# Optimization experiments

Hardware: AMD Instinct MI355X
Metric: run time of the kernel (lower is better)

## Reference

```python
import jax, jax.numpy as jnp
import numpy as np

K = 10
NUM_BLKS = 6
LN_EPS = 1e-6
NODE_D = 64


def layer_norm(x, g, b):
    m = jnp.mean(x, axis=-1, keepdims=True)
    v = jnp.var(x, axis=-1, keepdims=True)
    return (x - m) * jax.lax.rsqrt(v + LN_EPS) * g + b


def setup_inputs() -> dict:
    key = jax.random.key(0)
    B, N_c, N_t, D_S, D_F = 4, 4096, 1024, 3, 4
    D_IN = 4 + D_S + D_F  # obs-embed(4) + s + f
    ks = jax.random.split(key, 32)
    sc = 0.02
    inp = {
        "s_ctx": jax.random.normal(ks[0], (B, N_c, D_S), jnp.float32),
        "f_ctx": jax.random.normal(ks[1], (B, N_c, D_F), jnp.float32),
        "s_test": jax.random.normal(ks[2], (B, N_t, D_S), jnp.float32),
        "valid_lens_ctx": jax.random.randint(ks[3], (B,), N_c // 2, N_c + 1).astype(jnp.int32),
        # embed_obs: nn.Embed(2, 4)
        "emb_obs": jax.random.normal(ks[4], (2, 4), jnp.float32) * sc,
        # embed_all: MLP([256,128,64], gelu)
        "ea_W0": jax.random.normal(ks[5], (D_IN, 256), jnp.float32) * sc, "ea_b0": jnp.zeros((256,), jnp.float32),
        "ea_W1": jax.random.normal(ks[6], (256, 128), jnp.float32) * sc, "ea_b1": jnp.zeros((128,), jnp.float32),
        "ea_W2": jax.random.normal(ks[7], (128, NODE_D), jnp.float32) * sc, "ea_b2": jnp.zeros((NODE_D,), jnp.float32),
        # top-level LayerNorm
        "ln_g": jnp.ones((NODE_D,), jnp.float32), "ln_b": jnp.zeros((NODE_D,), jnp.float32),
        # GraphKRBlock params, stacked over NUM_BLKS blocks
        "blk_Wm0": jax.random.normal(ks[8], (NUM_BLKS, NODE_D + 1, 128), jnp.float32) * sc,
        "blk_bm0": jnp.zeros((NUM_BLKS, 128), jnp.float32),
        "blk_Wm1": jax.random.normal(ks[9], (NUM_BLKS, 128, NODE_D), jnp.float32) * sc,
        "blk_bm1": jnp.zeros((NUM_BLKS, NODE_D), jnp.float32),
        "blk_Wu0": jax.random.normal(ks[10], (NUM_BLKS, 2 * NODE_D, 128), jnp.float32) * sc,
        "blk_bu0": jnp.zeros((NUM_BLKS, 128), jnp.float32),
        "blk_Wu1": jax.random.normal(ks[11], (NUM_BLKS, 128, NODE_D), jnp.float32) * sc,
        "blk_bu1": jnp.zeros((NUM_BLKS, NODE_D), jnp.float32),
        "blk_lng": jnp.ones((NUM_BLKS, NODE_D), jnp.float32),
        "blk_lnb": jnp.zeros((NUM_BLKS, NODE_D), jnp.float32),
        # head: MLP([256,64,2], gelu)
        "hd_W0": jax.random.normal(ks[12], (NODE_D, 256), jnp.float32) * sc, "hd_b0": jnp.zeros((256,), jnp.float32),
        "hd_W1": jax.random.normal(ks[13], (256, 64), jnp.float32) * sc, "hd_b1": jnp.zeros((64,), jnp.float32),
        "hd_W2": jax.random.normal(ks[14], (64, 2), jnp.float32) * sc, "hd_b2": jnp.zeros((2,), jnp.float32),
    }
    return inp


def reference(s_ctx, f_ctx, s_test, valid_lens_ctx,
              emb_obs, ea_W0, ea_b0, ea_W1, ea_b1, ea_W2, ea_b2, ln_g, ln_b,
              blk_Wm0, blk_bm0, blk_Wm1, blk_bm1, blk_Wu0, blk_bu0, blk_Wu1, blk_bu1,
              blk_lng, blk_lnb, hd_W0, hd_b0, hd_W1, hd_b1, hd_W2, hd_b2):
    B, N_c, _ = s_ctx.shape
    N_t = s_test.shape[1]

    # --- per-sample O(n^2) KNN graph build (custom_k_nearest_senders, l2 dist) ---
    mask = jnp.arange(N_c)[None, :] < valid_lens_ctx[:, None]          # [B,N_c]
    s_send = jnp.where(mask[..., None], s_ctx, 1e6)                    # invalid -> far away
    rx = jnp.concatenate([s_ctx, s_test], axis=1)                      # [B,N,d_s] receivers
    d = jnp.sqrt(jnp.sum((rx[:, :, None, :] - s_send[:, None, :, :]) ** 2, axis=-1))  # [B,N,N_c]
    negd, senders = jax.lax.top_k(-d, K)                               # k-nearest: [B,N,K]
    dists = -negd                                                       # ascending distances

    # --- embeddings: stack(embed_obs, s, f) -> embed_all MLP -> LayerNorm ---
    def embed(x):
        h = jax.nn.gelu(x @ ea_W0 + ea_b0)
        h = jax.nn.gelu(h @ ea_W1 + ea_b1)
        h = h @ ea_W2 + ea_b2
        return layer_norm(h, ln_g, ln_b)

    ctx_in = jnp.concatenate(
        [jnp.broadcast_to(emb_obs[1], (B, N_c, emb_obs.shape[1])), s_ctx, f_ctx], axis=-1)
    test_in = jnp.concatenate(
        [jnp.broadcast_to(emb_obs[0], (B, N_t, emb_obs.shape[1])), s_test,
         jnp.zeros((B, N_t, f_ctx.shape[-1]), f_ctx.dtype)], axis=-1)
    nodes = jnp.concatenate([embed(ctx_in), embed(test_in)], axis=1)   # [B,N,64]

    # --- num_blks GraphKRBlock message-passing blocks ---
    bidx = jnp.arange(B)[:, None, None]
    w = jax.nn.softmax(-dists, axis=-1)                                # kernel weights per receiver
    for i in range(NUM_BLKS):
        sf = nodes[bidx, senders]                                      # gather senders [B,N,K,64]
        m_in = jnp.concatenate([sf, dists[..., None]], axis=-1)        # [B,N,K,65]
        m = jax.nn.gelu(m_in @ blk_Wm0[i] + blk_bm0[i]) @ blk_Wm1[i] + blk_bm1[i]
        agg = jnp.einsum('bnk,bnkd->bnd', w, m)                        # scatter-to-receivers
        u_in = jnp.concatenate([nodes, agg], axis=-1)                  # [B,N,128]
        upd = jax.nn.gelu(u_in @ blk_Wu0[i] + blk_bu0[i]) @ blk_Wu1[i] + blk_bu1[i]
        nodes = layer_norm(nodes + upd, blk_lng[i], blk_lnb[i])

    # --- head on test nodes ---
    x_t = nodes[:, N_c:, :]                                            # [B,N_t,64]
    h = jax.nn.gelu(x_t @ hd_W0 + hd_b0)
    h = jax.nn.gelu(h @ hd_W1 + hd_b1)
    f_dist = h @ hd_W2 + hd_b2                                         # [B,N_t,2]
    f_mu, f_log_var = jnp.split(f_dist, 2, axis=-1)
    f_std = jnp.exp(f_log_var / 2)                                     # min_std = 0.0
    return f_mu, f_std
```

## Files before the change

### kernel.cpp

```cpp
#include <hip/hip_runtime.h>
#include <math.h>

#define BB 4
#define NC 4096
#define NT 1024
#define NN (NC + NT)
#define NODES (BB * NN)
#define DD 64
#define KNN 10
#define NBLK 6
#define BIGF 3.0e38f
#define LM 5

typedef __attribute__((ext_vector_type(8))) short short8;
typedef __attribute__((ext_vector_type(4))) float f32x4;
typedef __attribute__((ext_vector_type(4))) int int4v;

__device__ __forceinline__ unsigned short f2bf(float f) {
    unsigned int u = __float_as_uint(f);
    unsigned int r = (u + 0x7fffu + ((u >> 16) & 1u)) >> 16;
    return (unsigned short)r;
}
__device__ __forceinline__ float bf2f(unsigned short h) {
    return __uint_as_float(((unsigned int)h) << 16);
}

__device__ __forceinline__ float gelu_f(float x) {
    const float c0 = 0.7978845608028654f;
    float x3 = x * x * x;
    float z2 = 2.0f * c0 * (x + 0.044715f * x3);
    float e = __expf(z2);
    float r = __builtin_amdgcn_rcpf(1.0f + e);
    return x - x * r;
}

__device__ __forceinline__ float wave_sum(float v) {
#pragma unroll
    for (int off = 32; off > 0; off >>= 1) v += __shfl_xor(v, off, 64);
    return v;
}

__device__ __forceinline__ f32x4 mfma_bf16(short8 a, short8 b, f32x4 c) {
    asm("v_mfma_f32_16x16x32_bf16 %0, %1, %2, %0" : "+v"(c) : "v"(a), "v"(b));
    return c;
}


__global__ __launch_bounds__(256) void k_convw(
    const float* __restrict__ Wm0, const float* __restrict__ Wm1,
    const float* __restrict__ Wu0, const float* __restrict__ Wu1,
    const float* __restrict__ bm0,
    const float* __restrict__ eW0, const float* __restrict__ eW1,
    const float* __restrict__ eW2,
    const float* __restrict__ hW0, const float* __restrict__ hW1,
    const float* __restrict__ sctx, const int* __restrict__ valid_lens,
    unsigned short* __restrict__ wtm0, unsigned short* __restrict__ wtm1p,
    unsigned short* __restrict__ wtu0, unsigned short* __restrict__ wtu1,
    float* __restrict__ wdp, float* __restrict__ bm0p,
    unsigned short* __restrict__ wte0, unsigned short* __restrict__ wte1,
    unsigned short* __restrict__ wte2,
    unsigned short* __restrict__ wth0, unsigned short* __restrict__ wth1,
    float4* __restrict__ s4)
{
    int t = blockIdx.x * 256 + threadIdx.x;
    if (t < 49152) {
        int i = t / 8192, r = t % 8192, n = r / 64, k = r % 64;
        wtm0[t] = f2bf(Wm0[(i * 65 + k) * 128 + n]);
    } else if (t < 98304) {
        int u = t - 49152;
        int i = u / 8192, r = u % 8192, n = r / 128, cp = r % 128;
        int col = ((cp & 7) << 4) | (cp >> 3);
        wtm1p[u] = f2bf(Wm1[(i * 128 + col) * 64 + n]);
    } else if (t < 196608) {
        int u = t - 98304;
        int i = u / 16384, r = u % 16384, n = r / 128, k = r % 128;
        wtu0[u] = f2bf(Wu0[(i * 128 + k) * 128 + n]);
    } else if (t < 245760) {
        int u = t - 196608;
        int i = u / 8192, r = u % 8192, n = r / 128, k = r % 128;
        wtu1[u] = f2bf(Wu1[(i * 128 + k) * 64 + n]);
    } else if (t < 246528) {
        int u = t - 245760;
        int i = u / 128, cp = u % 128;
        int col = ((cp & 7) << 4) | (cp >> 3);
        wdp[u] = Wm0[(i * 65 + 64) * 128 + col];
    } else if (t < 247296) {
        int u = t - 246528;
        int i = u / 128, cp = u % 128;
        int col = ((cp & 7) << 4) | (cp >> 3);
        bm0p[u] = bm0[i * 128 + col];
    } else if (t < 255488) {
        int u = t - 247296;
        int n = u / 32, k = u % 32;
        wte0[u] = (k < 11) ? f2bf(eW0[k * 256 + n]) : 0;
    } else if (t < 288256) {
        int u = t - 255488;
        int n = u / 256, k = u % 256;
        wte1[u] = f2bf(eW1[k * 128 + n]);
    } else if (t < 296448) {
        int u = t - 288256;
        int n = u / 128, k = u % 128;
        wte2[u] = f2bf(eW2[k * 64 + n]);
    } else if (t < 312832) {
        int u = t - 296448;
        int n = u / 64, k = u % 64;
        wth0[u] = f2bf(hW0[k * 256 + n]);
    } else if (t < 329216) {
        int u = t - 312832;
        int n = u / 256, k = u % 256;
        wth1[u] = f2bf(hW1[k * 64 + n]);
    } else if (t < 329216 + BB * NC) {
        int u = t - 329216;
        int b = u / NC, j = u % NC;
        bool ok = j < valid_lens[b];
        float x = ok ? sctx[u * 3] : 1.0e6f;
        float y = ok ? sctx[u * 3 + 1] : 1.0e6f;
        float z = ok ? sctx[u * 3 + 2] : 1.0e6f;
        s4[u] = make_float4(x, y, z, 0.0f);
    }
}

__global__ __launch_bounds__(256) void k_embed2(
    const float* __restrict__ s_ctx, const float* __restrict__ f_ctx,
    const float* __restrict__ s_test, const float* __restrict__ emb_obs,
    const unsigned short* __restrict__ WT0, const float* __restrict__ b0,
    const unsigned short* __restrict__ WT1, const float* __restrict__ b1,
    const unsigned short* __restrict__ WT2, const float* __restrict__ b2,
    const float* __restrict__ g, const float* __restrict__ bta,
    const unsigned short* __restrict__ Wm0n,
    unsigned short* __restrict__ nodes,
    unsigned short* __restrict__ Pout)
{
    __shared__ unsigned short H0[4][16 * 256];
    __shared__ unsigned short H1[4][16 * 128];
    __shared__ unsigned short XO[4][16 * 64];
    int t = threadIdx.x;
    int wave = t >> 6, lane = t & 63, lr = lane & 15, lk = lane >> 4;
    int rb = wave * 16;
    int n0 = blockIdx.x * 64;
    int bq = n0 / NN, nloc0 = n0 % NN;
    bool is_ctx = nloc0 < NC;
    int nr = nloc0 + rb + lr;
    float xv[8];
#pragma unroll
    for (int j = 0; j < 8; ++j) xv[j] = 0.0f;
    if (lk == 0) {
        const float* eb = emb_obs + (is_ctx ? 4 : 0);
        xv[0] = eb[0]; xv[1] = eb[1]; xv[2] = eb[2]; xv[3] = eb[3];
        if (is_ctx) {
            const float* sp = s_ctx + ((size_t)(bq * NC + nr)) * 3;
            const float* fp = f_ctx + ((size_t)(bq * NC + nr)) * 4;
            xv[4] = sp[0]; xv[5] = sp[1]; xv[6] = sp[2]; xv[7] = fp[0];
        } else {
            const float* sp = s_test + ((size_t)(bq * NT + nr - NC)) * 3;
            xv[4] = sp[0]; xv[5] = sp[1]; xv[6] = sp[2];
        }
    } else if (lk == 1 && is_ctx) {
        const float* fp = f_ctx + ((size_t)(bq * NC + nr)) * 4;
        xv[0] = fp[1]; xv[1] = fp[2]; xv[2] = fp[3];
    }
    short8 a;
#pragma unroll
    for (int j = 0; j < 8; ++j) a[j] = (short)f2bf(xv[j]);

    f32x4 acc0[16];
#pragma unroll
    for (int nt = 0; nt < 16; ++nt) {
        short8 bb = *(const short8*)(WT0 + (nt * 16 + lr) * 32 + lk * 8);
        f32x4 z = (f32x4){0.f, 0.f, 0.f, 0.f};
        acc0[nt] = mfma_bf16(a, bb, z);
    }
    unsigned short* h0 = &H0[wave][0];
#pragma unroll
    for (int nt = 0; nt < 16; ++nt) {
        int col = nt * 16 + lr;
        float bias = b0[col];
        int u = col >> 3;
#pragma unroll
        for (int j = 0; j < 4; ++j) {
            int row = lk * 4 + j;
            float v = gelu_f(acc0[nt][j] + bias);
            int us = (u & 16) | ((u ^ row) & 15);
            h0[row * 256 + us * 8 + (col & 7)] = f2bf(v);
        }
    }
    f32x4 acc1[8];
#pragma unroll
    for (int nt = 0; nt < 8; ++nt) acc1[nt] = (f32x4){0.f, 0.f, 0.f, 0.f};
#pragma unroll
    for (int ks = 0; ks < 8; ++ks) {
        int u = ks * 4 + lk;
        int us = (u & 16) | ((u ^ lr) & 15);
        short8 aa = *(const short8*)(&h0[lr * 256 + us * 8]);
#pragma unroll
        for (int nt = 0; nt < 8; ++nt) {
            short8 bb = *(const short8*)(WT1 + (nt * 16 + lr) * 256 + ks * 32 + lk * 8);
            acc1[nt] = mfma_bf16(aa, bb, acc1[nt]);
        }
    }
    unsigned short* h1 = &H1[wave][0];
#pragma unroll
    for (int nt = 0; nt < 8; ++nt) {
        int col = nt * 16 + lr;
        float bias = b1[col];
        int u = col >> 3;
#pragma unroll
        for (int j = 0; j < 4; ++j) {
            int row = lk * 4 + j;
            float v = gelu_f(acc1[nt][j] + bias);
            int us = (u ^ row) & 15;
            h1[row * 128 + us * 8 + (col & 7)] = f2bf(v);
        }
    }
    f32x4 acc2[4];
#pragma unroll
    for (int nt = 0; nt < 4; ++nt) acc2[nt] = (f32x4){0.f, 0.f, 0.f, 0.f};
#pragma unroll
    for (int ks = 0; ks < 4; ++ks) {
        int u = ks * 4 + lk;
        int us = (u ^ lr) & 15;
        short8 aa = *(const short8*)(&h1[lr * 128 + us * 8]);
#pragma unroll
        for (int nt = 0; nt < 4; ++nt) {
            short8 bb = *(const short8*)(WT2 + (nt * 16 + lr) * 128 + ks * 32 + lk * 8);
            acc2[nt] = mfma_bf16(aa, bb, acc2[nt]);
        }
    }
    float vals[4][4];
#pragma unroll
    for (int j = 0; j < 4; ++j)
#pragma unroll
        for (int nt = 0; nt < 4; ++nt)
            vals[j][nt] = acc2[nt][j] + b2[nt * 16 + lr];
    unsigned short* xo = &XO[wave][0];
#pragma unroll
    for (int j = 0; j < 4; ++j) {
        float s = vals[j][0] + vals[j][1] + vals[j][2] + vals[j][3];
#pragma unroll
        for (int m = 1; m < 16; m <<= 1) s += __shfl_xor(s, m, 64);
        float mean = s * (1.0f / 64.0f);
        float vs = 0.0f;
#pragma unroll
        for (int nt = 0; nt < 4; ++nt) { float d = vals[j][nt] - mean; vs += d * d; }
#pragma unroll
        for (int m = 1; m < 16; m <<= 1) vs += __shfl_xor(vs, m, 64);
        float inv = rsqrtf(vs * (1.0f / 64.0f) + 1e-6f);
        int row = lk * 4 + j;
        int node = n0 + rb + row;
#pragma unroll
        for (int nt = 0; nt < 4; ++nt) {
            int col = nt * 16 + lr;
            float o = (vals[j][nt] - mean) * inv * g[col] + bta[col];
            unsigned short ob = f2bf(o);
            nodes[(size_t)node * 64 + col] = ob;
            xo[row * 64 + ((col >> 3) ^ (row & 7)) * 8 + (col & 7)] = ob;
        }
    }
    f32x4 accP[8];
#pragma unroll
    for (int nt = 0; nt < 8; ++nt) accP[nt] = (f32x4){0.f, 0.f, 0.f, 0.f};
#pragma unroll
    for (int ks = 0; ks < 2; ++ks) {
        short8 aa = *(const short8*)(&xo[lr * 64 + ((ks * 4 + lk) ^ (lr & 7)) * 8]);
#pragma unroll
        for (int nt = 0; nt < 8; ++nt) {
            short8 bb = *(const short8*)(Wm0n + (nt * 16 + lr) * 64 + ks * 32 + lk * 8);
            accP[nt] = mfma_bf16(aa, bb, accP[nt]);
        }
    }
#pragma unroll
    for (int j = 0; j < 4; ++j) {
        int node = n0 + rb + lk * 4 + j;
        short8 ps;
#pragma unroll
        for (int nt = 0; nt < 8; ++nt) ps[nt] = (short)f2bf(accP[nt][j]);
        *(short8*)(Pout + (size_t)node * 128 + lr * 8) = ps;
    }
}

__global__ __launch_bounds__(256) void k_topk(
    const float4* __restrict__ s4, const float* __restrict__ s_ctx,
    const float* __restrict__ s_test,
    float* __restrict__ dists, int* __restrict__ senders, float* __restrict__ wout)
{
    __shared__ float cd[4 * 64 * 11];
    __shared__ float slotv[4][4][16];
    __shared__ int   sloti[4][4][16];
    __shared__ int   cnt[4][4];
    int wave = threadIdx.x >> 6;
    int lane = threadIdx.x & 63;
    int r0 = blockIdx.x * 16 + wave * 4;
    int b = r0 / NN;
    const float4* sc = s4 + (size_t)b * NC;
    float px[4], py[4], pz[4];
#pragma unroll
    for (int q = 0; q < 4; ++q) {
        int n = (r0 + q) % NN;
        const float* p = (n < NC) ? &s_ctx[(size_t)(b * NC + n) * 3]
                                  : &s_test[(size_t)(b * NT + (n - NC)) * 3];
        px[q] = p[0]; py[q] = p[1]; pz[q] = p[2];
    }
    float bq[4][LM];
#pragma unroll
    for (int q = 0; q < 4; ++q)
#pragma unroll
        for (int k = 0; k < LM; ++k) bq[q][k] = BIGF;
#pragma unroll 8
    for (int i = 0; i < 64; ++i) {
        int j = lane + (i << 6);
        float4 s = sc[j];
#pragma unroll
        for (int q = 0; q < 4; ++q) {
            float dx = px[q] - s.x, dy = py[q] - s.y, dz = pz[q] - s.z;
            float d2 = fmaf(dx, dx, fmaf(dy, dy, dz * dz));
#pragma unroll
            for (int k = LM - 1; k >= 1; --k)
                bq[q][k] = __builtin_amdgcn_fmed3f(bq[q][k - 1], bq[q][k], d2);
            bq[q][0] = fminf(bq[q][0], d2);
        }
    }
    int base = (wave * 64 + lane) * 11;
    float T[4];
#pragma unroll
    for (int q = 0; q < 4; ++q) {
#pragma unroll
        for (int k = 0; k < LM; ++k) cd[base + k] = bq[q][k];
        cd[base + LM] = BIGF;
        __builtin_amdgcn_wave_barrier();
        int head = 0;
        float Tl = BIGF;
#pragma unroll
        for (int rr = 0; rr < KNN; ++rr) {
            float v = cd[base + head];
            float mv = v;
#pragma unroll
            for (int off = 32; off > 0; off >>= 1) mv = fminf(mv, __shfl_xor(mv, off, 64));
            unsigned long long ball = __ballot(v == mv);
            int win = __ffsll(ball) - 1;
            if (lane == win) head++;
            Tl = mv;
        }
        T[q] = Tl;
    }
    if (lane < 4) cnt[wave][lane] = 0;
    __builtin_amdgcn_wave_barrier();
#pragma unroll 4
    for (int i = 0; i < 64; ++i) {
        int j = lane + (i << 6);
        float4 s = sc[j];
#pragma unroll
        for (int q = 0; q < 4; ++q) {
            float dx = px[q] - s.x, dy = py[q] - s.y, dz = pz[q] - s.z;
            float v = fmaf(dx, dx, fmaf(dy, dy, dz * dz));
            if (v <= T[q]) {
                int slot = atomicAdd(&cnt[wave][q], 1);
                if (slot < 16) { slotv[wave][q][slot] = v; sloti[wave][q][slot] = j; }
            }
        }
    }
    __builtin_amdgcn_wave_barrier();
#pragma unroll
    for (int q = 0; q < 4; ++q) {
        int count = cnt[wave][q];
        if (count > 16) count = 16;
        float e = 0.0f, d = 0.0f;
        int isel = 0, rank = 0;
        bool own = lane < count;
        if (own) {
            float myv = slotv[wave][q][lane];
            int myi = sloti[wave][q][lane];
            for (int j = 0; j < count; ++j) {
                float vj = slotv[wave][q][j];
                int ij = sloti[wave][q][j];
                rank += (vj < myv || (vj == myv && ij < myi)) ? 1 : 0;
            }
            own = rank < KNN;
            if (own) {
                isel = myi;
                d = sqrtf(myv);
                e = __expf(-d);
            }
        }
        float ssum = wave_sum(e);
        if (own) {
            size_t o = (size_t)(r0 + q) * KNN + rank;
            dists[o] = d;
            senders[o] = isel;
            wout[o] = e / ssum;
        }
    }
}

__global__ __launch_bounds__(256) void k_blk(
    const unsigned short* __restrict__ nodes_in,
    const unsigned short* __restrict__ P,
    const float* __restrict__ dists, const int* __restrict__ senders,
    const float* __restrict__ w,
    const float* __restrict__ wdp, const float* __restrict__ bm0p,
    const unsigned short* __restrict__ Wm1p,
    const float* __restrict__ bm1,
    const unsigned short* __restrict__ WTu0,
    const float* __restrict__ bu0,
    const unsigned short* __restrict__ WTu1,
    const float* __restrict__ bu1,
    const float* __restrict__ lng, const float* __restrict__ lnb,
    const unsigned short* __restrict__ Wm0n,
    const int doP,
    unsigned short* __restrict__ nodes_out,
    unsigned short* __restrict__ Pout,
    const int doHead, const int testOnly,
    const unsigned short* __restrict__ wth0,
    const float* __restrict__ hb0,
    const unsigned short* __restrict__ wth1,
    const float* __restrict__ hb1,
    const float* __restrict__ hW2, const float* __restrict__ hb2,
    float* __restrict__ out)
{
    __shared__ unsigned short X[16 * 64];
    __shared__ unsigned short G[16 * 128];
    __shared__ unsigned short AG[16 * 64];
    __shared__ unsigned short H[16 * 128];
    __shared__ unsigned short XO[16 * 64];
    __shared__ float VF[16 * 65];
    __shared__ unsigned short HH[16 * 256];
    __shared__ unsigned short HH1[16 * 72];
    __shared__ int   sidE[160];
    __shared__ float dE[160], wE[160];
    int l = threadIdx.x;
    int wave = l >> 6, lane = l & 63;
    int bid = blockIdx.x;
    int tile = testOnly ? ((bid >> 6) * 320 + 256 + (bid & 63))
                        : ((bid & 7) * 160 + (bid >> 3));
    int n0 = tile * 16;
    int b = n0 / NN;
    size_t bbase = (size_t)b * NN;
    int e0 = n0 * KNN;
    if (l < 160) {
        sidE[l] = senders[e0 + l];
        dE[l]   = dists[e0 + l];
        wE[l]   = w[e0 + l];
    }
    if (l < 128) {
        int row = l >> 3, u = l & 7;
        int4v v = *(const int4v*)(nodes_in + ((size_t)(n0 + row)) * 64 + u * 8);
        *(int4v*)(&X[row * 64 + (u ^ (row & 7)) * 8]) = v;
    }
    __syncthreads();
    float wd0 = wdp[2 * lane], wd1 = wdp[2 * lane + 1];
    float bb0 = bm0p[2 * lane], bb1 = bm0p[2 * lane + 1];
    const unsigned int* Pb = (const unsigned int*)P;
    unsigned int* G32 = (unsigned int*)G;
#pragma unroll
    for (int nn = 0; nn < 4; ++nn) {
        int n = wave * 4 + nn;
        float a0 = 0.0f, a1 = 0.0f;
#pragma unroll
        for (int k = 0; k < KNN; ++k) {
            int e = n * KNN + k;
            int sid = sidE[e];
            float dd = dE[e], ww = wE[e];
            unsigned int pr = Pb[(bbase + sid) * 64 + lane];
            float p0 = __uint_as_float(pr << 16);
            float p1 = __uint_as_float(pr & 0xFFFF0000u);
            float g0 = gelu_f(fmaf(dd, wd0, p0 + bb0));
            float g1 = gelu_f(fmaf(dd, wd1, p1 + bb1));
            a0 = fmaf(ww, g0, a0);
            a1 = fmaf(ww, g1, a1);
        }
        unsigned int pk = (unsigned int)f2bf(a0) | ((unsigned int)f2bf(a1) << 16);
        G32[n * 64 + ((lane >> 2) ^ n) * 4 + (lane & 3)] = pk;
    }
    __syncthreads();
    int lr = lane & 15, lk = lane >> 4;
    if (wave < 2) {
        f32x4 accA[2];
#pragma unroll
        for (int n2 = 0; n2 < 2; ++n2) accA[n2] = (f32x4){0.f, 0.f, 0.f, 0.f};
#pragma unroll
        for (int ks = 0; ks < 4; ++ks) {
            short8 a = *(const short8*)(&G[lr * 128 + ((ks * 4 + lk) ^ lr) * 8]);
#pragma unroll
            for (int n2 = 0; n2 < 2; ++n2) {
                int nt = wave * 2 + n2;
                short8 bb = *(const short8*)(Wm1p + (nt * 16 + lr) * 128 + ks * 32 + lk * 8);
                accA[n2] = mfma_bf16(a, bb, accA[n2]);
            }
        }
#pragma unroll
        for (int n2 = 0; n2 < 2; ++n2) {
            int col = (wave * 2 + n2) * 16 + lr;
            float bias = bm1[col];
#pragma unroll
            for (int j = 0; j < 4; ++j) {
                int row = lk * 4 + j;
                AG[row * 64 + ((col >> 3) ^ (row & 7)) * 8 + (col & 7)] =
                    f2bf(accA[n2][j] + bias);
            }
        }
    }
    __syncthreads();
    if (wave < 2) {
        f32x4 acc[4];
#pragma unroll
        for (int n4 = 0; n4 < 4; ++n4) acc[n4] = (f32x4){0.f, 0.f, 0.f, 0.f};
#pragma unroll
        for (int ks = 0; ks < 4; ++ks) {
            short8 a;
            if (ks < 2) a = *(const short8*)(&X[lr * 64 + ((ks * 4 + lk) ^ (lr & 7)) * 8]);
            else        a = *(const short8*)(&AG[lr * 64 + (((ks - 2) * 4 + lk) ^ (lr & 7)) * 8]);
#pragma unroll
            for (int n4 = 0; n4 < 4; ++n4) {
                int nt = wave * 4 + n4;
                short8 bb = *(const short8*)(WTu0 + (nt * 16 + lr) * 128 + ks * 32 + lk * 8);
                acc[n4] = mfma_bf16(a, bb, acc[n4]);
            }
        }
#pragma unroll
        for (int n4 = 0; n4 < 4; ++n4) {
            int col = (wave * 4 + n4) * 16 + lr;
            float bias = bu0[col];
#pragma unroll
            for (int j = 0; j < 4; ++j) {
                int lrow = lk * 4 + j;
                float v = gelu_f(acc[n4][j] + bias);
                H[lrow * 128 + ((col >> 3) ^ lrow) * 8 + (col & 7)] = f2bf(v);
            }
        }
    }
    __syncthreads();
    if (wave < 2) {
        f32x4 acc2[2];
#pragma unroll
        for (int n2 = 0; n2 < 2; ++n2) acc2[n2] = (f32x4){0.f, 0.f, 0.f, 0.f};
#pragma unroll
        for (int ks = 0; ks < 4; ++ks) {
            short8 a = *(const short8*)(&H[lr * 128 + ((ks * 4 + lk) ^ lr) * 8]);
#pragma unroll
            for (int n2 = 0; n2 < 2; ++n2) {
                int nt = wave * 2 + n2;
                short8 bb = *(const short8*)(WTu1 + (nt * 16 + lr) * 128 + ks * 32 + lk * 8);
                acc2[n2] = mfma_bf16(a, bb, acc2[n2]);
            }
        }
#pragma unroll
        for (int n2 = 0; n2 < 2; ++n2) {
            int col = (wave * 2 + n2) * 16 + lr;
            float bias = bu1[col];
#pragma unroll
            for (int j = 0; j < 4; ++j) {
                int row = lk * 4 + j;
                float x = bf2f(X[row * 64 + ((col >> 3) ^ (row & 7)) * 8 + (col & 7)]);
                VF[row * 65 + col] = x + acc2[n2][j] + bias;
            }
        }
    }
    __syncthreads();
    if (wave == 0) {
        float vals[4][4];
#pragma unroll
        for (int j = 0; j < 4; ++j) {
            int row = lk * 4 + j;
#pragma unroll
            for (int nt = 0; nt < 4; ++nt)
                vals[j][nt] = VF[row * 65 + nt * 16 + lr];
        }
#pragma unroll
        for (int j = 0; j < 4; ++j) {
            int row = lk * 4 + j;
            float s = vals[j][0] + vals[j][1] + vals[j][2] + vals[j][3];
#pragma unroll
            for (int mm = 1; mm < 16; mm <<= 1) s += __shfl_xor(s, mm, 64);
            float mean = s * (1.0f / 64.0f);
            float vs = 0.0f;
#pragma unroll
            for (int nt = 0; nt < 4; ++nt) { float d = vals[j][nt] - mean; vs += d * d; }
#pragma unroll
            for (int mm = 1; mm < 16; mm <<= 1) vs += __shfl_xor(vs, mm, 64);
            float inv = rsqrtf(vs * (1.0f / 64.0f) + 1e-6f);
#pragma unroll
            for (int nt = 0; nt < 4; ++nt) {
                int col = nt * 16 + lr;
                float o = (vals[j][nt] - mean) * inv * lng[col] + lnb[col];
                unsigned short ob = f2bf(o);
                nodes_out[((size_t)(n0 + row)) * 64 + col] = ob;
                XO[row * 64 + ((col >> 3) ^ (row & 7)) * 8 + (col & 7)] = ob;
            }
        }
    }
    __syncthreads();
    if (doP && wave == 1) {
        f32x4 accP[8];
#pragma unroll
        for (int nt = 0; nt < 8; ++nt) accP[nt] = (f32x4){0.f, 0.f, 0.f, 0.f};
#pragma unroll
        for (int ks = 0; ks < 2; ++ks) {
            short8 aa = *(const short8*)(&XO[lr * 64 + ((ks * 4 + lk) ^ (lr & 7)) * 8]);
#pragma unroll
            for (int nt = 0; nt < 8; ++nt) {
                short8 bb = *(const short8*)(Wm0n + (nt * 16 + lr) * 64 + ks * 32 + lk * 8);
                accP[nt] = mfma_bf16(aa, bb, accP[nt]);
            }
        }
#pragma unroll
        for (int j = 0; j < 4; ++j) {
            int node = n0 + lk * 4 + j;
            short8 ps;
#pragma unroll
            for (int nt = 0; nt < 8; ++nt) ps[nt] = (short)f2bf(accP[nt][j]);
            *(short8*)(Pout + (size_t)node * 128 + lr * 8) = ps;
        }
    }
    if (doHead && wave == 0) {
        int nloc = n0 % NN;
        int bq = n0 / NN;
#pragma unroll
        for (int half = 0; half < 2; ++half) {
            f32x4 ah[8];
#pragma unroll
            for (int nt = 0; nt < 8; ++nt) ah[nt] = (f32x4){0.f, 0.f, 0.f, 0.f};
#pragma unroll
            for (int ks = 0; ks < 2; ++ks) {
                short8 aa = *(const short8*)(&XO[lr * 64 + ((ks * 4 + lk) ^ (lr & 7)) * 8]);
#pragma unroll
                for (int nt = 0; nt < 8; ++nt) {
                    int col16 = half * 8 + nt;
                    short8 bb = *(const short8*)(wth0 + (col16 * 16 + lr) * 64 + ks * 32 + lk * 8);
                    ah[nt] = mfma_bf16(aa, bb, ah[nt]);
                }
            }
#pragma unroll
            for (int nt = 0; nt < 8; ++nt) {
                int col = (half * 8 + nt) * 16 + lr;
                float bias = hb0[col];
                int u = col >> 3;
#pragma unroll
                for (int j = 0; j < 4; ++j) {
                    int row = lk * 4 + j;
                    float v = gelu_f(ah[nt][j] + bias);
                    int us = (u & 16) | ((u ^ row) & 15);
                    HH[row * 256 + us * 8 + (col & 7)] = f2bf(v);
                }
            }
        }
        f32x4 a1h[4];
#pragma unroll
        for (int nt = 0; nt < 4; ++nt) a1h[nt] = (f32x4){0.f, 0.f, 0.f, 0.f};
#pragma unroll
        for (int ks = 0; ks < 8; ++ks) {
            int u = ks * 4 + lk;
            int us = (u & 16) | ((u ^ lr) & 15);
            short8 aa = *(const short8*)(&HH[lr * 256 + us * 8]);
#pragma unroll
            for (int nt = 0; nt < 4; ++nt) {
                short8 bb = *(const short8*)(wth1 + (nt * 16 + lr) * 256 + ks * 32 + lk * 8);
                a1h[nt] = mfma_bf16(aa, bb, a1h[nt]);
            }
        }
#pragma unroll
        for (int nt = 0; nt < 4; ++nt) {
            int col = nt * 16 + lr;
            float bias = hb1[col];
#pragma unroll
            for (int j = 0; j < 4; ++j) {
                int row = lk * 4 + j;
                HH1[row * 72 + col] = f2bf(gelu_f(a1h[nt][j] + bias));
            }
        }
        int task = lane >> 1;
        int row = task >> 1;
        int o = task & 1;
        int t2 = lane & 1;
        float pp = 0.0f;
#pragma unroll
        for (int d = 0; d < 32; ++d) {
            int dd = t2 * 32 + d;
            pp += bf2f(HH1[row * 72 + dd]) * hW2[dd * 2 + o];
        }
        pp += __shfl_xor(pp, 1, 64);
        if (t2 == 0) {
            int gg = bq * NT + (nloc - NC) + row;
            if (o == 0) out[gg] = pp + hb2[0];
            else        out[BB * NT + gg] = __expf(0.5f * (pp + hb2[1]));
        }
    }
}

extern "C" void kernel_launch(void* const* d_in, const int* in_sizes, int n_in,
                              void* d_out, int out_size, void* d_ws, size_t ws_size,
                              hipStream_t stream)
{
    (void)in_sizes; (void)n_in; (void)out_size; (void)ws_size;
    const float* s_ctx   = (const float*)d_in[0];
    const float* f_ctx   = (const float*)d_in[1];
    const float* s_test  = (const float*)d_in[2];
    const int*   valid   = (const int*)d_in[3];
    const float* emb_obs = (const float*)d_in[4];
    const float* ea_W0   = (const float*)d_in[5];
    const float* ea_b0   = (const float*)d_in[6];
    const float* ea_W1   = (const float*)d_in[7];
    const float* ea_b1   = (const float*)d_in[8];
    const float* ea_W2   = (const float*)d_in[9];
    const float* ea_b2   = (const float*)d_in[10];
    const float* ln_g    = (const float*)d_in[11];
    const float* ln_b    = (const float*)d_in[12];
    const float* blk_Wm0 = (const float*)d_in[13];
    const float* blk_bm0 = (const float*)d_in[14];
    const float* blk_Wm1 = (const float*)d_in[15];
    const float* blk_bm1 = (const float*)d_in[16];
    const float* blk_Wu0 = (const float*)d_in[17];
    const float* blk_bu0 = (const float*)d_in[18];
    const float* blk_Wu1 = (const float*)d_in[19];
    const float* blk_bu1 = (const float*)d_in[20];
    const float* blk_lng = (const float*)d_in[21];
    const float* blk_lnb = (const float*)d_in[22];
    const float* hd_W0   = (const float*)d_in[23];
    const float* hd_b0   = (const float*)d_in[24];
    const float* hd_W1   = (const float*)d_in[25];
    const float* hd_b1   = (const float*)d_in[26];
    const float* hd_W2   = (const float*)d_in[27];
    const float* hd_b2   = (const float*)d_in[28];

    char* p = (char*)d_ws;
    auto alloc = [&](size_t bytes) { char* r = p; p += (bytes + 255) & ~(size_t)255; return r; };
    unsigned short* nodesA = (unsigned short*)alloc((size_t)NODES * 64 * 2);
    unsigned short* nodesB = (unsigned short*)alloc((size_t)NODES * 64 * 2);
    unsigned short* PA     = (unsigned short*)alloc((size_t)NODES * 128 * 2);
    unsigned short* PB     = (unsigned short*)alloc((size_t)NODES * 128 * 2);
    float* dists   = (float*)alloc((size_t)NODES * KNN * 4);
    float* wbuf    = (float*)alloc((size_t)NODES * KNN * 4);
    int*   senders = (int*)alloc((size_t)NODES * KNN * 4);
    unsigned short* wtm0  = (unsigned short*)alloc((size_t)6 * 8192 * 2);
    unsigned short* wtm1p = (unsigned short*)alloc((size_t)6 * 8192 * 2);
    unsigned short* wtu0  = (unsigned short*)alloc((size_t)6 * 16384 * 2);
    unsigned short* wtu1  = (unsigned short*)alloc((size_t)6 * 8192 * 2);
    float* wdp  = (float*)alloc((size_t)6 * 128 * 4);
    float* bm0p = (float*)alloc((size_t)6 * 128 * 4);
    unsigned short* wte0 = (unsigned short*)alloc((size_t)8192 * 2);
    unsigned short* wte1 = (unsigned short*)alloc((size_t)32768 * 2);
    unsigned short* wte2 = (unsigned short*)alloc((size_t)8192 * 2);
    unsigned short* wth0 = (unsigned short*)alloc((size_t)16384 * 2);
    unsigned short* wth1 = (unsigned short*)alloc((size_t)16384 * 2);
    float4* s4 = (float4*)alloc((size_t)BB * NC * 16);

    k_convw<<<1350, 256, 0, stream>>>(
        blk_Wm0, blk_Wm1, blk_Wu0, blk_Wu1, blk_bm0,
        ea_W0, ea_W1, ea_W2, hd_W0, hd_W1, s_ctx, valid,
        wtm0, wtm1p, wtu0, wtu1, wdp, bm0p, wte0, wte1, wte2, wth0, wth1, s4);

    k_embed2<<<NODES / 64, 256, 0, stream>>>(s_ctx, f_ctx, s_test, emb_obs,
        wte0, ea_b0, wte1, ea_b1, wte2, ea_b2, ln_g, ln_b, wtm0, nodesA, PA);

    k_topk<<<NODES / 16, 256, 0, stream>>>(s4, s_ctx, s_test,
                                           dists, senders, wbuf);

    unsigned short* nin = nodesA; unsigned short* nout = nodesB;
    unsigned short* pin = PA;     unsigned short* pout = PB;
    for (int i = 0; i < NBLK; ++i) {
        int doP = (i < NBLK - 1) ? 1 : 0;
        int doHead = (i == NBLK - 1) ? 1 : 0;
        int testOnly = doHead;
        int grid = testOnly ? (BB * NT / 16) : (NODES / 16);
        const unsigned short* wm0n = wtm0 + (size_t)((i + 1) % NBLK) * 8192;
        k_blk<<<grid, 256, 0, stream>>>(nin, pin, dists, senders, wbuf,
            wdp + (size_t)i * 128, bm0p + (size_t)i * 128,
            wtm1p + (size_t)i * 8192, blk_bm1 + (size_t)i * 64,
            wtu0 + (size_t)i * 16384, blk_bu0 + (size_t)i * 128,
            wtu1 + (size_t)i * 8192, blk_bu1 + (size_t)i * 64,
            blk_lng + (size_t)i * 64, blk_lnb + (size_t)i * 64,
            wm0n, doP, nout, pout,
            doHead, testOnly, wth0, hd_b0, wth1, hd_b1, hd_W2, hd_b2, (float*)d_out);
        unsigned short* tmp = nin; nin = nout; nout = tmp;
        tmp = pin; pin = pout; pout = tmp;
    }
}
```

Measured before the change: 267.5 us.

## Shrink embed blocks to one wave and spread block MLP tiles across all waves

The embed kernel now launches one 64-thread wave per 16-node block instead of four waves per 64 nodes, so each block uses less LDS and more blocks can be scheduled. In the per-layer block kernel, the message-output, update-hidden and update-output GEMM stages previously ran on only two of four waves. They are now divided across all four waves, each taking one or two 16-column tiles. The aim is to cut idle waves and shorten the serialized MFMA chains, at the cost of more per-wave weight loads and more blocks to schedule.

New measurement: 248.2 us (median of 2 runs). 1.08x faster.

```diff
diff --git a/kernel.cpp b/kernel.cpp
--- a/kernel.cpp
+++ b/kernel.cpp
@@ -120,7 +120,7 @@
     }
 }
 
-__global__ __launch_bounds__(256) void k_embed2(
+__global__ __launch_bounds__(64) void k_embed2(
     const float* __restrict__ s_ctx, const float* __restrict__ f_ctx,
     const float* __restrict__ s_test, const float* __restrict__ emb_obs,
     const unsigned short* __restrict__ WT0, const float* __restrict__ b0,
@@ -131,16 +131,14 @@
     unsigned short* __restrict__ nodes,
     unsigned short* __restrict__ Pout)
 {
-    __shared__ unsigned short H0[4][16 * 256];
-    __shared__ unsigned short H1[4][16 * 128];
-    __shared__ unsigned short XO[4][16 * 64];
-    int t = threadIdx.x;
-    int wave = t >> 6, lane = t & 63, lr = lane & 15, lk = lane >> 4;
-    int rb = wave * 16;
-    int n0 = blockIdx.x * 64;
+    __shared__ unsigned short h0[16 * 256];
+    __shared__ unsigned short h1[16 * 128];
+    __shared__ unsigned short xo[16 * 64];
+    int lane = threadIdx.x & 63, lr = lane & 15, lk = lane >> 4;
+    int n0 = blockIdx.x * 16;
     int bq = n0 / NN, nloc0 = n0 % NN;
     bool is_ctx = nloc0 < NC;
-    int nr = nloc0 + rb + lr;
+    int nr = nloc0 + lr;
     float xv[8];
 #pragma unroll
     for (int j = 0; j < 8; ++j) xv[j] = 0.0f;
@@ -170,7 +168,6 @@
         f32x4 z = (f32x4){0.f, 0.f, 0.f, 0.f};
         acc0[nt] = mfma_bf16(a, bb, z);
     }
-    unsigned short* h0 = &H0[wave][0];
 #pragma unroll
     for (int nt = 0; nt < 16; ++nt) {
         int col = nt * 16 + lr;
@@ -198,7 +195,6 @@
             acc1[nt] = mfma_bf16(aa, bb, acc1[nt]);
         }
     }
-    unsigned short* h1 = &H1[wave][0];
 #pragma unroll
     for (int nt = 0; nt < 8; ++nt) {
         int col = nt * 16 + lr;
@@ -232,7 +228,6 @@
 #pragma unroll
         for (int nt = 0; nt < 4; ++nt)
             vals[j][nt] = acc2[nt][j] + b2[nt * 16 + lr];
-    unsigned short* xo = &XO[wave][0];
 #pragma unroll
     for (int j = 0; j < 4; ++j) {
         float s = vals[j][0] + vals[j][1] + vals[j][2] + vals[j][3];
@@ -246,7 +241,7 @@
         for (int m = 1; m < 16; m <<= 1) vs += __shfl_xor(vs, m, 64);
         float inv = rsqrtf(vs * (1.0f / 64.0f) + 1e-6f);
         int row = lk * 4 + j;
-        int node = n0 + rb + row;
+        int node = n0 + row;
 #pragma unroll
         for (int nt = 0; nt < 4; ++nt) {
             int col = nt * 16 + lr;
@@ -270,7 +265,7 @@
     }
 #pragma unroll
     for (int j = 0; j < 4; ++j) {
-        int node = n0 + rb + lk * 4 + j;
+        int node = n0 + lk * 4 + j;
         short8 ps;
 #pragma unroll
         for (int nt = 0; nt < 8; ++nt) ps[nt] = (short)f2bf(accP[nt][j]);
@@ -472,86 +467,70 @@
     }
     __syncthreads();
     int lr = lane & 15, lk = lane >> 4;
-    if (wave < 2) {
-        f32x4 accA[2];
-#pragma unroll
-        for (int n2 = 0; n2 < 2; ++n2) accA[n2] = (f32x4){0.f, 0.f, 0.f, 0.f};
+    {
+        f32x4 accA = (f32x4){0.f, 0.f, 0.f, 0.f};
+        int nt = wave;
 #pragma unroll
         for (int ks = 0; ks < 4; ++ks) {
             short8 a = *(const short8*)(&G[lr * 128 + ((ks * 4 + lk) ^ lr) * 8]);
-#pragma unroll
-            for (int n2 = 0; n2 < 2; ++n2) {
-                int nt = wave * 2 + n2;
-                short8 bb = *(const short8*)(Wm1p + (nt * 16 + lr) * 128 + ks * 32 + lk * 8);
-                accA[n2] = mfma_bf16(a, bb, accA[n2]);
-            }
-        }
-#pragma unroll
-        for (int n2 = 0; n2 < 2; ++n2) {
-            int col = (wave * 2 + n2) * 16 + lr;
-            float bias = bm1[col];
-#pragma unroll
-            for (int j = 0; j < 4; ++j) {
-                int row = lk * 4 + j;
-                AG[row * 64 + ((col >> 3) ^ (row & 7)) * 8 + (col & 7)] =
-                    f2bf(accA[n2][j] + bias);
-            }
+            short8 bb = *(const short8*)(Wm1p + (nt * 16 + lr) * 128 + ks * 32 + lk * 8);
+            accA = mfma_bf16(a, bb, accA);
+        }
+        int col = nt * 16 + lr;
+        float bias = bm1[col];
+#pragma unroll
+        for (int j = 0; j < 4; ++j) {
+            int row = lk * 4 + j;
+            AG[row * 64 + ((col >> 3) ^ (row & 7)) * 8 + (col & 7)] =
+                f2bf(accA[j] + bias);
         }
     }
     __syncthreads();
-    if (wave < 2) {
-        f32x4 acc[4];
-#pragma unroll
-        for (int n4 = 0; n4 < 4; ++n4) acc[n4] = (f32x4){0.f, 0.f, 0.f, 0.f};
+    {
+        f32x4 acc[2];
+#pragma unroll
+        for (int n2 = 0; n2 < 2; ++n2) acc[n2] = (f32x4){0.f, 0.f, 0.f, 0.f};
 #pragma unroll
         for (int ks = 0; ks < 4; ++ks) {
             short8 a;
             if (ks < 2) a = *(const short8*)(&X[lr * 64 + ((ks * 4 + lk) ^ (lr & 7)) * 8]);
             else        a = *(const short8*)(&AG[lr * 64 + (((ks - 2) * 4 + lk) ^ (lr & 7)) * 8]);
 #pragma unroll
-            for (int n4 = 0; n4 < 4; ++n4) {
-                int nt = wave * 4 + n4;
+            for (int n2 = 0; n2 < 2; ++n2) {
+                int nt = wave * 2 + n2;
                 short8 bb = *(const short8*)(WTu0 + (nt * 16 + lr) * 128 + ks * 32 + lk * 8);
-                acc[n4] = mfma_bf16(a, bb, acc[n4]);
-            }
-        }
-#pragma unroll
-        for (int n4 = 0; n4 < 4; ++n4) {
-            int col = (wave * 4 + n4) * 16 + lr;
+                acc[n2] = mfma_bf16(a, bb, acc[n2]);
+            }
+        }
+#pragma unroll
+        for (int n2 = 0; n2 < 2; ++n2) {
+            int col = (wave * 2 + n2) * 16 + lr;
             float bias = bu0[col];
 #pragma unroll
             for (int j = 0; j < 4; ++j) {
                 int lrow = lk * 4 + j;
-                float v = gelu_f(acc[n4][j] + bias);
+                float v = gelu_f(acc[n2][j] + bias);
                 H[lrow * 128 + ((col >> 3) ^ lrow) * 8 + (col & 7)] = f2bf(v);
             }
         }
     }
     __syncthreads();
-    if (wave < 2) {
-        f32x4 acc2[2];
-#pragma unroll
-        for (int n2 = 0; n2 < 2; ++n2) acc2[n2] = (f32x4){0.f, 0.f, 0.f, 0.f};
+    {
+        f32x4 acc2 = (f32x4){0.f, 0.f, 0.f, 0.f};
+        int nt = wave;
 #pragma unroll
         for (int ks = 0; ks < 4; ++ks) {
             short8 a = *(const short8*)(&H[lr * 128 + ((ks * 4 + lk) ^ lr) * 8]);
-#pragma unroll
-            for (int n2 = 0; n2 < 2; ++n2) {
-                int nt = wave * 2 + n2;
-                short8 bb = *(const short8*)(WTu1 + (nt * 16 + lr) * 128 + ks * 32 + lk * 8);
-                acc2[n2] = mfma_bf16(a, bb, acc2[n2]);
-            }
-        }
-#pragma unroll
-        for (int n2 = 0; n2 < 2; ++n2) {
-            int col = (wave * 2 + n2) * 16 + lr;
-            float bias = bu1[col];
-#pragma unroll
-            for (int j = 0; j < 4; ++j) {
-                int row = lk * 4 + j;
-                float x = bf2f(X[row * 64 + ((col >> 3) ^ (row & 7)) * 8 + (col & 7)]);
-                VF[row * 65 + col] = x + acc2[n2][j] + bias;
-            }
+            short8 bb = *(const short8*)(WTu1 + (nt * 16 + lr) * 128 + ks * 32 + lk * 8);
+            acc2 = mfma_bf16(a, bb, acc2);
+        }
+        int col = nt * 16 + lr;
+        float bias = bu1[col];
+#pragma unroll
+        for (int j = 0; j < 4; ++j) {
+            int row = lk * 4 + j;
+            float x = bf2f(X[row * 64 + ((col >> 3) ^ (row & 7)) * 8 + (col & 7)]);
+            VF[row * 65 + col] = x + acc2[j] + bias;
         }
     }
     __syncthreads();
@@ -747,7 +726,7 @@
         ea_W0, ea_W1, ea_W2, hd_W0, hd_W1, s_ctx, valid,
         wtm0, wtm1p, wtu0, wtu1, wdp, bm0p, wte0, wte1, wte2, wth0, wth1, s4);
 
-    k_embed2<<<NODES / 64, 256, 0, stream>>>(s_ctx, f_ctx, s_test, emb_obs,
+    k_embed2<<<NODES / 16, 64, 0, stream>>>(s_ctx, f_ctx, s_test, emb_obs,
         wte0, ea_b0, wte1, ea_b1, wte2, ea_b2, ln_g, ln_b, wtm0, nodesA, PA);
 
     k_topk<<<NODES / 16, 256, 0, stream>>>(s4, s_ctx, s_test,
```
